# Kernel optimization log

Measured on AMD Instinct MI355X. Metric: run time of the kernel, lower is better.

The kernel has to match this reference:

```python
import jax, jax.numpy as jnp
import numpy as np

B, L, D, H, VOCAB = 8, 1024, 1024, 8, 32000
DH = D // H  # dim_per_head = 128
SCALE = float((DH // H) ** (-0.5))  # faithful to key.size(-1)//num_heads
EPS = 1e-5


def setup_inputs() -> dict:
    key = jax.random.key(0)
    ks = jax.random.split(key, 12)
    tokens = jax.random.randint(ks[0], (B, L), 0, VOCAB)
    s = 0.02
    emb = jax.random.normal(ks[1], (VOCAB, D), jnp.float32) * s
    emb = emb.at[0].set(0.0)  # padding_idx=0
    Wq = jax.random.normal(ks[2], (D, D), jnp.float32) * s
    Wk = jax.random.normal(ks[3], (D, D), jnp.float32) * s
    Wv = jax.random.normal(ks[4], (D, D), jnp.float32) * s
    Wo = jax.random.normal(ks[5], (D, D), jnp.float32) * s
    bq = jnp.zeros((D,), jnp.float32)
    bk = jnp.zeros((D,), jnp.float32)
    bv = jnp.zeros((D,), jnp.float32)
    bo = jnp.zeros((D,), jnp.float32)
    gamma = jnp.ones((2 * D,), jnp.float32)
    beta = jnp.zeros((2 * D,), jnp.float32)
    return {"tokens": tokens, "emb": emb, "Wq": Wq, "bq": bq, "Wk": Wk,
            "bk": bk, "Wv": Wv, "bv": bv, "Wo": Wo, "bo": bo,
            "gamma": gamma, "beta": beta}


def reference(tokens, emb, Wq, bq, Wk, bk, Wv, bv, Wo, bo, gamma, beta):
    # padding mask: [B, L, L] True where key token == 0
    pad = (tokens == 0)  # [B, L]
    mask = jnp.broadcast_to(pad[:, None, :], (B, L, L))
    mask = jnp.tile(mask, (H, 1, 1))  # torch .repeat(num_heads,1,1) -> [H*B, L, L]

    x = emb[tokens]  # [B, L, D]

    q = (x @ Wq + bq).reshape(B * H, L, DH)  # faithful interleaved view
    k = (x @ Wk + bk).reshape(B * H, L, DH)
    v = (x @ Wv + bv).reshape(B * H, L, DH)

    scores = jnp.einsum('bqd,bkd->bqk', q, k) * SCALE
    scores = jnp.where(mask, -jnp.inf, scores)
    attn = jax.nn.softmax(scores, axis=-1)
    ctx = jnp.einsum('bqk,bkd->bqd', attn, v).reshape(B, L, D)

    out = ctx @ Wo + bo  # [B, L, D]
    r = x + out
    maxpool = r.max(axis=1)   # [B, D]
    meanpool = r.mean(axis=1)  # [B, D]
    agg = jnp.concatenate([maxpool, meanpool], axis=1)  # [B, 2D]

    mu = agg.mean(axis=-1, keepdims=True)
    var = agg.var(axis=-1, keepdims=True)
    return (agg - mu) / jnp.sqrt(var + EPS) * gamma + beta
```

## Files before the change

### kernel.cpp

```cpp
#include <hip/hip_runtime.h>
#include <math.h>

typedef __attribute__((ext_vector_type(8))) short short8;
typedef __attribute__((ext_vector_type(4))) float f32x4;

constexpr int CB = 8, CL = 1024, CD = 1024, CDH = 128, CM = 8192;
constexpr float CSCALE = 0.25f;
constexpr float CEPS = 1e-5f;

__device__ inline ushort f2b(float f) {
    union { float f; unsigned u; } v; v.f = f;
    unsigned r = v.u + 0x7FFF + ((v.u >> 16) & 1);
    return (ushort)(r >> 16);
}
__device__ inline float b2f(ushort u) {
    union { unsigned u; float f; } v; v.u = ((unsigned)u) << 16;
    return v.f;
}

__device__ inline void gld16(const void* g, void* l) {
    __builtin_amdgcn_global_load_lds(
        (const __attribute__((address_space(1))) void*)g,
        (__attribute__((address_space(3))) void*)l, 16, 0, 0);
}

__global__ __launch_bounds__(256) void k_gather(const int* __restrict__ tokens,
                                                const float* __restrict__ emb,
                                                float* __restrict__ x,
                                                ushort* __restrict__ xb) {
    int row = blockIdx.x;
    int tok = tokens[row];
    float4 v = ((const float4*)(emb + (size_t)tok * CD))[threadIdx.x];
    ((float4*)(x + (size_t)row * CD))[threadIdx.x] = v;
    ushort4 o; o.x = f2b(v.x); o.y = f2b(v.y); o.z = f2b(v.z); o.w = f2b(v.w);
    ((ushort4*)(xb + (size_t)row * CD))[threadIdx.x] = o;
}

__global__ __launch_bounds__(256) void k_wtrans(const float* __restrict__ W,
                                                ushort* __restrict__ Wt) {
    __shared__ float ws_[32][33];
    const int tk = blockIdx.x * 32, tn = blockIdx.y * 32;
    const int t = threadIdx.x;
    {
        int r = t >> 3, c4 = (t & 7) * 4;
        *(float4*)&ws_[r][c4] = *(const float4*)&W[(size_t)(tk + r) * CD + tn + c4];
    }
    __syncthreads();
    int n = t >> 3, k4 = (t & 7) * 4;
    ushort4 o;
    o.x = f2b(ws_[k4 + 0][n]); o.y = f2b(ws_[k4 + 1][n]);
    o.z = f2b(ws_[k4 + 2][n]); o.w = f2b(ws_[k4 + 3][n]);
    *(ushort4*)&Wt[(size_t)(tn + n) * CD + tk + k4] = o;
}

__global__ __launch_bounds__(256) void k_gemm_qkv(const ushort* __restrict__ A,
                                                  const ushort* __restrict__ Wt3,
                                                  const float* __restrict__ b0,
                                                  const float* __restrict__ b1,
                                                  const float* __restrict__ b2,
                                                  ushort* __restrict__ C3) {
    __shared__ ushort As[128 * 32];
    __shared__ ushort Bs[128 * 32];
    const int z = blockIdx.z;
    const ushort* Bt  = Wt3 + (size_t)z * CD * CD;
    const float* bias = (z == 0) ? b0 : ((z == 1) ? b1 : b2);
    ushort* Cout      = C3 + (size_t)z * CM * CD;

    const int t = threadIdx.x, w = t >> 6, l = t & 63;
    const int lane15 = l & 15, quad = l >> 4;
    const int bm = blockIdx.y * 128, bn = blockIdx.x * 128;
    const int wm = (w >> 1) * 64, wn = (w & 1) * 64;
    const int arow = l >> 2;
    const int aseg = (l & 3) * 8;
    f32x4 acc[4][4] = {};

    for (int k0 = 0; k0 < CD; k0 += 32) {
        __syncthreads();
        #pragma unroll
        for (int c2 = 0; c2 < 2; ++c2) {
            int c = w * 2 + c2;
            gld16(A  + (size_t)(bm + c * 16 + arow) * CD + k0 + aseg, &As[c * 512 + l * 8]);
            gld16(Bt + (size_t)(bn + c * 16 + arow) * CD + k0 + aseg, &Bs[c * 512 + l * 8]);
        }
        __syncthreads();
        short8 af[4], bf[4];
        #pragma unroll
        for (int im = 0; im < 4; ++im)
            af[im] = *(const short8*)&As[(wm + im * 16 + lane15) * 32 + quad * 8];
        #pragma unroll
        for (int in = 0; in < 4; ++in)
            bf[in] = *(const short8*)&Bs[(wn + in * 16 + lane15) * 32 + quad * 8];
        #pragma unroll
        for (int im = 0; im < 4; ++im)
            #pragma unroll
            for (int in = 0; in < 4; ++in)
                acc[im][in] = __builtin_amdgcn_mfma_f32_16x16x32_bf16(af[im], bf[in], acc[im][in], 0, 0, 0);
    }
    #pragma unroll
    for (int in = 0; in < 4; ++in) {
        int col = bn + wn + in * 16 + lane15;
        float bv = bias[col];
        #pragma unroll
        for (int im = 0; im < 4; ++im) {
            int row0 = bm + wm + im * 16 + quad * 4;
            #pragma unroll
            for (int r = 0; r < 4; ++r)
                Cout[(size_t)(row0 + r) * CD + col] = f2b(acc[im][in][r] + bv);
        }
    }
}

__global__ __launch_bounds__(256) void k_gemm_out(const ushort* __restrict__ A,
                                                  const ushort* __restrict__ Bt,
                                                  const float* __restrict__ bias,
                                                  const float* __restrict__ resid,
                                                  float* __restrict__ Cout) {
    __shared__ ushort As[128 * 32];
    __shared__ ushort Bs[128 * 32];
    const int t = threadIdx.x, w = t >> 6, l = t & 63;
    const int lane15 = l & 15, quad = l >> 4;
    const int bm = blockIdx.y * 128, bn = blockIdx.x * 128;
    const int wm = (w >> 1) * 64, wn = (w & 1) * 64;
    const int arow = l >> 2;
    const int aseg = (l & 3) * 8;
    f32x4 acc[4][4] = {};

    for (int k0 = 0; k0 < CD; k0 += 32) {
        __syncthreads();
        #pragma unroll
        for (int c2 = 0; c2 < 2; ++c2) {
            int c = w * 2 + c2;
            gld16(A  + (size_t)(bm + c * 16 + arow) * CD + k0 + aseg, &As[c * 512 + l * 8]);
            gld16(Bt + (size_t)(bn + c * 16 + arow) * CD + k0 + aseg, &Bs[c * 512 + l * 8]);
        }
        __syncthreads();
        short8 af[4], bf[4];
        #pragma unroll
        for (int im = 0; im < 4; ++im)
            af[im] = *(const short8*)&As[(wm + im * 16 + lane15) * 32 + quad * 8];
        #pragma unroll
        for (int in = 0; in < 4; ++in)
            bf[in] = *(const short8*)&Bs[(wn + in * 16 + lane15) * 32 + quad * 8];
        #pragma unroll
        for (int im = 0; im < 4; ++im)
            #pragma unroll
            for (int in = 0; in < 4; ++in)
                acc[im][in] = __builtin_amdgcn_mfma_f32_16x16x32_bf16(af[im], bf[in], acc[im][in], 0, 0, 0);
    }
    #pragma unroll
    for (int in = 0; in < 4; ++in) {
        int col = bn + wn + in * 16 + lane15;
        float bv = bias[col];
        #pragma unroll
        for (int im = 0; im < 4; ++im) {
            int row0 = bm + wm + im * 16 + quad * 4;
            #pragma unroll
            for (int r = 0; r < 4; ++r) {
                size_t idx = (size_t)(row0 + r) * CD + col;
                Cout[idx] = acc[im][in][r] + bv + resid[idx];
            }
        }
    }
}

__global__ __launch_bounds__(256) void k_vtransp(const ushort* __restrict__ v,
                                                 ushort* __restrict__ Vtp) {
    __shared__ ushort Vs[64 * 136];
    const int i = blockIdx.x >> 4, kt = blockIdx.x & 15;
    const ushort* src = v + (size_t)i * 131072 + (size_t)kt * 64 * 128;
    const int t = threadIdx.x;
    #pragma unroll
    for (int ii = 0; ii < 4; ++ii) {
        int idx = t + 256 * ii;
        int key = idx >> 4, seg = idx & 15;
        *(uint4*)&Vs[key * 136 + seg * 8] = *(const uint4*)&src[key * 128 + seg * 8];
    }
    __syncthreads();
    ushort* dst = Vtp + (size_t)blockIdx.x * 8192;
    #pragma unroll
    for (int it = 0; it < 4; ++it) {
        int L = t + 256 * it;
        int cell = L & 63;
        int quadk = cell >> 4, l15 = cell & 15;
        int p = L >> 6;
        int d = (p >> 1) * 16 + l15;
        int kb = ((p & 1) * 4 + quadk) * 8;
        uint pk[4];
        #pragma unroll
        for (int jj = 0; jj < 4; ++jj) {
            uint lo = Vs[(kb + 2 * jj) * 136 + d];
            uint hi = Vs[(kb + 2 * jj + 1) * 136 + d];
            pk[jj] = lo | (hi << 16);
        }
        *(uint4*)&dst[(size_t)L * 8] = *(uint4*)pk;
    }
}

__global__ __launch_bounds__(512) void k_attn(const ushort* __restrict__ Q,
                                              const ushort* __restrict__ K,
                                              const ushort* __restrict__ Vtp,
                                              const int* __restrict__ tokens,
                                              ushort* __restrict__ ctx) {
    __shared__ ushort Ks[16 * 512];
    __shared__ ushort Vs[16 * 512];
    __shared__ ushort Ps[8 * 1088];
    __shared__ ushort Msk[CL];
    const int i = blockIdx.x, qb = blockIdx.y * 128;
    const int t = threadIdx.x, w = t >> 6, l = t & 63;
    const int lane15 = l & 15, quad = l >> 4;

    {
        const int* tokb = tokens + (i & 7) * CL;
        #pragma unroll
        for (int jj = 0; jj < 2; ++jj) {
            int idx = t + 512 * jj;
            Msk[idx] = (tokb[idx] == 0) ? (ushort)0xFF80 : (ushort)0;
        }
    }
    const int qrow = qb + w * 16 + lane15;
    short8 af[4];
    #pragma unroll
    for (int kc = 0; kc < 4; ++kc)
        af[kc] = *(const short8*)&Q[(size_t)i * 131072 + (size_t)qrow * 128 + kc * 32 + quad * 8];

    f32x4 oacc[8];
    #pragma unroll
    for (int dt = 0; dt < 8; ++dt) oacc[dt] = f32x4{0.f, 0.f, 0.f, 0.f};
    float lsum[4] = {0.f, 0.f, 0.f, 0.f};
    const int wbase = w * 1088;

    for (int kt = 0; kt < 16; ++kt) {
        __syncthreads();
        #pragma unroll
        for (int c = 0; c < 2; ++c) {
            int p = w * 2 + c;
            gld16(K + (size_t)i * 131072 + (size_t)(kt * 64 + (p >> 2) * 16 + lane15) * 128
                    + (p & 3) * 32 + quad * 8,
                  &Ks[p * 512 + l * 8]);
            gld16(Vtp + ((size_t)(i * 16 + kt) * 16 + p) * 512 + l * 8,
                  &Vs[p * 512 + l * 8]);
        }
        __syncthreads();

        f32x4 sc[4];
        #pragma unroll
        for (int j = 0; j < 4; ++j) {
            sc[j] = f32x4{0.f, 0.f, 0.f, 0.f};
            #pragma unroll
            for (int kc = 0; kc < 4; ++kc) {
                short8 bk = *(const short8*)&Ks[(j * 4 + kc) * 512 + l * 8];
                sc[j] = __builtin_amdgcn_mfma_f32_16x16x32_bf16(af[kc], bk, sc[j], 0, 0, 0);
            }
        }
        #pragma unroll
        for (int j = 0; j < 4; ++j) {
            float mj = b2f(Msk[kt * 64 + j * 16 + lane15]);
            #pragma unroll
            for (int r = 0; r < 4; ++r) {
                float p = __expf(fmaf(sc[j][r], CSCALE, mj));
                sc[j][r] = p;
                lsum[r] += p;
            }
        }
        #pragma unroll
        for (int j = 0; j < 4; ++j) {
            int ks2 = j >> 1;
            int qq  = (j & 1) * 2 + (lane15 >> 3);
            int pos = lane15 & 7;
            #pragma unroll
            for (int r = 0; r < 4; ++r) {
                union { float f; unsigned u; } cv; cv.f = sc[j][r];
                Ps[wbase + ks2 * 544 + qq * 136 + (quad * 4 + r) * 8 + pos] =
                    (ushort)(cv.u >> 16);
            }
        }
        short8 ap[2];
        #pragma unroll
        for (int ks2 = 0; ks2 < 2; ++ks2)
            ap[ks2] = *(const short8*)&Ps[wbase + ks2 * 544 + quad * 136 + lane15 * 8];
        #pragma unroll
        for (int dt = 0; dt < 8; ++dt)
            #pragma unroll
            for (int ks2 = 0; ks2 < 2; ++ks2) {
                short8 bv = *(const short8*)&Vs[(dt * 2 + ks2) * 512 + l * 8];
                oacc[dt] = __builtin_amdgcn_mfma_f32_16x16x32_bf16(ap[ks2], bv, oacc[dt], 0, 0, 0);
            }
    }
    float inv[4];
    #pragma unroll
    for (int r = 0; r < 4; ++r) {
        float s = lsum[r];
        #pragma unroll
        for (int off = 1; off < 16; off <<= 1) s += __shfl_xor(s, off);
        inv[r] = 1.f / s;
    }
    #pragma unroll
    for (int dt = 0; dt < 8; ++dt)
        #pragma unroll
        for (int r = 0; r < 4; ++r) {
            int q = qb + w * 16 + quad * 4 + r;
            ctx[(size_t)i * 131072 + (size_t)q * 128 + dt * 16 + lane15] =
                f2b(oacc[dt][r] * inv[r]);
        }
}

__global__ __launch_bounds__(256) void k_pool1(const float* __restrict__ R,
                                               float* __restrict__ pmax,
                                               float* __restrict__ psum) {
    const int chunk = blockIdx.x, b = blockIdx.y;
    const int d4 = threadIdx.x;
    const float4* base = (const float4*)(R + ((size_t)b * CL + chunk * 32) * CD) + d4;
    float4 mx = base[0];
    float4 sm = mx;
    for (int lr = 1; lr < 32; ++lr) {
        float4 v = base[(size_t)lr * (CD / 4)];
        mx.x = fmaxf(mx.x, v.x); mx.y = fmaxf(mx.y, v.y);
        mx.z = fmaxf(mx.z, v.z); mx.w = fmaxf(mx.w, v.w);
        sm.x += v.x; sm.y += v.y; sm.z += v.z; sm.w += v.w;
    }
    size_t off = ((size_t)b * 32 + chunk) * CD;
    ((float4*)(pmax + off))[d4] = mx;
    ((float4*)(psum + off))[d4] = sm;
}

__global__ __launch_bounds__(1024) void k_pool2(const float* __restrict__ pmax,
                                                const float* __restrict__ psum,
                                                const float* __restrict__ gamma,
                                                const float* __restrict__ beta,
                                                float* __restrict__ out) {
    __shared__ float rs[16], rq[16];
    __shared__ float s_mu, s_inv;
    const int b = blockIdx.x;
    const int d = threadIdx.x;
    float mx = -3.4e38f, sm = 0.f;
    for (int c = 0; c < 32; ++c) {
        size_t off = ((size_t)b * 32 + c) * CD + d;
        mx = fmaxf(mx, pmax[off]);
        sm += psum[off];
    }
    const float a0 = mx;
    const float a1 = sm * (1.0f / 1024.0f);
    float s = a0 + a1;
    float qd = a0 * a0 + a1 * a1;
    #pragma unroll
    for (int off = 32; off > 0; off >>= 1) {
        s  += __shfl_xor(s, off);
        qd += __shfl_xor(qd, off);
    }
    const int wid = d >> 6;
    if ((d & 63) == 0) { rs[wid] = s; rq[wid] = qd; }
    __syncthreads();
    if (d == 0) {
        float S = 0.f, Qm = 0.f;
        for (int ww = 0; ww < 16; ++ww) { S += rs[ww]; Qm += rq[ww]; }
        float mu  = S * (1.0f / 2048.0f);
        float var = Qm * (1.0f / 2048.0f) - mu * mu;
        s_mu = mu; s_inv = 1.0f / sqrtf(var + CEPS);
    }
    __syncthreads();
    const float mu = s_mu, inv = s_inv;
    out[(size_t)b * 2048 + d]        = (a0 - mu) * inv * gamma[d]        + beta[d];
    out[(size_t)b * 2048 + 1024 + d] = (a1 - mu) * inv * gamma[1024 + d] + beta[1024 + d];
}

extern "C" void kernel_launch(void* const* d_in, const int* in_sizes, int n_in,
                              void* d_out, int out_size, void* d_ws, size_t ws_size,
                              hipStream_t stream) {
    const int*   tokens = (const int*)d_in[0];
    const float* emb    = (const float*)d_in[1];
    const float* Wq     = (const float*)d_in[2];
    const float* bq     = (const float*)d_in[3];
    const float* Wk     = (const float*)d_in[4];
    const float* bk     = (const float*)d_in[5];
    const float* Wv     = (const float*)d_in[6];
    const float* bv     = (const float*)d_in[7];
    const float* Wo     = (const float*)d_in[8];
    const float* bo     = (const float*)d_in[9];
    const float* gamma  = (const float*)d_in[10];
    const float* beta   = (const float*)d_in[11];
    float* out = (float*)d_out;

    char* p = (char*)d_ws;
    float*  x   = (float*)p;   p += (size_t)CM * CD * 4;
    ushort* xb  = (ushort*)p;  p += (size_t)CM * CD * 2;
    ushort* wqt = (ushort*)p;  p += (size_t)CD * CD * 2;
    ushort* wkt = (ushort*)p;  p += (size_t)CD * CD * 2;
    ushort* wvt = (ushort*)p;  p += (size_t)CD * CD * 2;
    ushort* wot = (ushort*)p;  p += (size_t)CD * CD * 2;
    ushort* qb_ = (ushort*)p;  p += (size_t)CM * CD * 2;
    ushort* kb_ = (ushort*)p;  p += (size_t)CM * CD * 2;
    ushort* vb_ = (ushort*)p;  p += (size_t)CM * CD * 2;
    ushort* Vtp = (ushort*)p;  p += (size_t)CM * CD * 2;
    float*  pmax = (float*)p;  p += (size_t)CB * 32 * CD * 4;
    float*  psum = (float*)p;  p += (size_t)CB * 32 * CD * 4;
    float*  R   = (float*)qb_;
    ushort* ctx = vb_;

    k_gather<<<CM, 256, 0, stream>>>(tokens, emb, x, xb);

    dim3 wg(32, 32);
    k_wtrans<<<wg, 256, 0, stream>>>(Wq, wqt);
    k_wtrans<<<wg, 256, 0, stream>>>(Wk, wkt);
    k_wtrans<<<wg, 256, 0, stream>>>(Wv, wvt);
    k_wtrans<<<wg, 256, 0, stream>>>(Wo, wot);

    dim3 gq(CD / 128, CM / 128, 3);
    k_gemm_qkv<<<gq, 256, 0, stream>>>(xb, wqt, bq, bk, bv, qb_);

    k_vtransp<<<64 * 16, 256, 0, stream>>>(vb_, Vtp);

    dim3 ag(64, 8);
    k_attn<<<ag, 512, 0, stream>>>(qb_, kb_, Vtp, tokens, ctx);

    dim3 gg(CD / 128, CM / 128);
    k_gemm_out<<<gg, 256, 0, stream>>>(ctx, wot, bo, x, R);

    k_pool1<<<dim3(32, CB), 256, 0, stream>>>(R, pmax, psum);
    k_pool2<<<CB, 1024, 0, stream>>>(pmax, psum, gamma, beta, out);
}
```

Before: 383.0 us.

## Pipeline GEMMs with double-buffered LDS and fuse pooling into output GEMM

Both GEMMs move to 256x128 tiles with 512 threads, a double-buffered LDS pipeline that prefetches the next K slice while MFMAs run, and setprio around the MFMA block. The QKV GEMM flattens the z dimension into blockIdx.x, which relies on the three transposed weights being contiguous in memory. The output GEMM now reduces max and sum over its rows in the epilogue, so the fp32 residual tensor R is never written and pool1 is removed. The cost is more LDS and registers per block and hand-written waitcnt/barrier sequencing that has to be exactly right.

```diff
diff --git a/kernel.cpp b/kernel.cpp
--- a/kernel.cpp
+++ b/kernel.cpp
@@ -53,56 +53,89 @@
     *(ushort4*)&Wt[(size_t)(tn + n) * CD + tk + k4] = o;
 }
 
-__global__ __launch_bounds__(256) void k_gemm_qkv(const ushort* __restrict__ A,
-                                                  const ushort* __restrict__ Wt3,
-                                                  const float* __restrict__ b0,
-                                                  const float* __restrict__ b1,
-                                                  const float* __restrict__ b2,
-                                                  ushort* __restrict__ C3) {
-    __shared__ ushort As[128 * 32];
-    __shared__ ushort Bs[128 * 32];
-    const int z = blockIdx.z;
-    const ushort* Bt  = Wt3 + (size_t)z * CD * CD;
-    const float* bias = (z == 0) ? b0 : ((z == 1) ? b1 : b2);
-    ushort* Cout      = C3 + (size_t)z * CM * CD;
-
+__device__ inline void stage24(const ushort* __restrict__ A,
+                               const ushort* __restrict__ B,
+                               ushort* ldsA, ushort* ldsB,
+                               int bm, int bn, int kbase,
+                               int w, int lane15, int quad, int l) {
+    #pragma unroll
+    for (int c = 0; c < 3; ++c) {
+        int pid = w * 3 + c;
+        if (pid < 16)
+            gld16(A + (size_t)(bm + pid * 16 + lane15) * CD + kbase + quad * 8,
+                  ldsA + pid * 512 + (size_t)l * 8);
+        else
+            gld16(B + (size_t)(bn + (pid - 16) * 16 + lane15) * CD + kbase + quad * 8,
+                  ldsB + (pid - 16) * 512 + (size_t)l * 8);
+    }
+}
+
+#define GEMM_PIPELINE(Aptr, Bptr)                                                  \
+    f32x4 acc[4][4] = {};                                                          \
+    stage24(Aptr, Bptr, &As_[0][0][0][0], &Bs_[0][0][0][0], bm, bn, 0,             \
+            w, lane15, quad, l);                                                   \
+    stage24(Aptr, Bptr, &As_[0][1][0][0], &Bs_[0][1][0][0], bm, bn, 32,            \
+            w, lane15, quad, l);                                                   \
+    asm volatile("s_waitcnt vmcnt(3)" ::: "memory");                               \
+    __builtin_amdgcn_s_barrier();                                                  \
+    int cur = 0;                                                                   \
+    for (int kt = 0; kt < 16; ++kt) {                                              \
+        const int nk = (kt + 1) & 15;                                              \
+        _Pragma("unroll")                                                          \
+        for (int kh = 0; kh < 2; ++kh) {                                           \
+            short8 af[4], bf[4];                                                   \
+            _Pragma("unroll")                                                      \
+            for (int im = 0; im < 4; ++im)                                         \
+                af[im] = *(const short8*)&As_[cur][kh][wr * 4 + im][(size_t)l * 8];\
+            _Pragma("unroll")                                                      \
+            for (int in = 0; in < 4; ++in)                                         \
+                bf[in] = *(const short8*)&Bs_[cur][kh][wc * 4 + in][(size_t)l * 8];\
+            stage24(Aptr, Bptr, &As_[cur ^ 1][kh][0][0], &Bs_[cur ^ 1][kh][0][0],  \
+                    bm, bn, nk * 64 + kh * 32, w, lane15, quad, l);                \
+            __builtin_amdgcn_s_barrier();                                          \
+            asm volatile("s_waitcnt lgkmcnt(0)" ::: "memory");                     \
+            __builtin_amdgcn_s_setprio(1);                                         \
+            _Pragma("unroll")                                                      \
+            for (int im = 0; im < 4; ++im)                                         \
+                _Pragma("unroll")                                                  \
+                for (int in = 0; in < 4; ++in)                                     \
+                    acc[im][in] = __builtin_amdgcn_mfma_f32_16x16x32_bf16(         \
+                        af[im], bf[in], acc[im][in], 0, 0, 0);                     \
+            __builtin_amdgcn_s_setprio(0);                                         \
+            asm volatile("s_waitcnt vmcnt(3)" ::: "memory");                       \
+            __builtin_amdgcn_s_barrier();                                          \
+        }                                                                          \
+        cur ^= 1;                                                                  \
+    }                                                                              \
+    asm volatile("s_waitcnt vmcnt(0)" ::: "memory");
+
+__global__ __launch_bounds__(512, 2) void k_gemm_qkv(const ushort* __restrict__ A,
+                                                     const ushort* __restrict__ Wt3,
+                                                     const float* __restrict__ b0,
+                                                     const float* __restrict__ b1,
+                                                     const float* __restrict__ b2,
+                                                     ushort* __restrict__ C3) {
+    __shared__ ushort As_[2][2][16][512];
+    __shared__ ushort Bs_[2][2][8][512];
     const int t = threadIdx.x, w = t >> 6, l = t & 63;
     const int lane15 = l & 15, quad = l >> 4;
-    const int bm = blockIdx.y * 128, bn = blockIdx.x * 128;
-    const int wm = (w >> 1) * 64, wn = (w & 1) * 64;
-    const int arow = l >> 2;
-    const int aseg = (l & 3) * 8;
-    f32x4 acc[4][4] = {};
-
-    for (int k0 = 0; k0 < CD; k0 += 32) {
-        __syncthreads();
-        #pragma unroll
-        for (int c2 = 0; c2 < 2; ++c2) {
-            int c = w * 2 + c2;
-            gld16(A  + (size_t)(bm + c * 16 + arow) * CD + k0 + aseg, &As[c * 512 + l * 8]);
-            gld16(Bt + (size_t)(bn + c * 16 + arow) * CD + k0 + aseg, &Bs[c * 512 + l * 8]);
-        }
-        __syncthreads();
-        short8 af[4], bf[4];
-        #pragma unroll
-        for (int im = 0; im < 4; ++im)
-            af[im] = *(const short8*)&As[(wm + im * 16 + lane15) * 32 + quad * 8];
-        #pragma unroll
-        for (int in = 0; in < 4; ++in)
-            bf[in] = *(const short8*)&Bs[(wn + in * 16 + lane15) * 32 + quad * 8];
-        #pragma unroll
-        for (int im = 0; im < 4; ++im)
-            #pragma unroll
-            for (int in = 0; in < 4; ++in)
-                acc[im][in] = __builtin_amdgcn_mfma_f32_16x16x32_bf16(af[im], bf[in], acc[im][in], 0, 0, 0);
-    }
+    const int wr = w >> 1, wc = w & 1;
+    const int bx = blockIdx.x, by = blockIdx.y;
+    const int bm = by * 256, bn = bx * 128;
+
+    GEMM_PIPELINE(A, Wt3)
+
+    const int z = bx >> 3;
+    const float* bias = (z == 0) ? b0 : ((z == 1) ? b1 : b2);
+    ushort* Cout = C3 + (size_t)z * CM * CD;
+    const int colbase = (bx & 7) * 128 + wc * 64;
     #pragma unroll
     for (int in = 0; in < 4; ++in) {
-        int col = bn + wn + in * 16 + lane15;
+        int col = colbase + in * 16 + lane15;
         float bv = bias[col];
         #pragma unroll
         for (int im = 0; im < 4; ++im) {
-            int row0 = bm + wm + im * 16 + quad * 4;
+            int row0 = bm + wr * 64 + im * 16 + quad * 4;
             #pragma unroll
             for (int r = 0; r < 4; ++r)
                 Cout[(size_t)(row0 + r) * CD + col] = f2b(acc[im][in][r] + bv);
@@ -110,56 +143,65 @@
     }
 }
 
-__global__ __launch_bounds__(256) void k_gemm_out(const ushort* __restrict__ A,
-                                                  const ushort* __restrict__ Bt,
-                                                  const float* __restrict__ bias,
-                                                  const float* __restrict__ resid,
-                                                  float* __restrict__ Cout) {
-    __shared__ ushort As[128 * 32];
-    __shared__ ushort Bs[128 * 32];
+__global__ __launch_bounds__(512, 2) void k_gemm_out(const ushort* __restrict__ A,
+                                                     const ushort* __restrict__ Bt,
+                                                     const float* __restrict__ bias,
+                                                     const float* __restrict__ resid,
+                                                     float* __restrict__ pmax,
+                                                     float* __restrict__ psum) {
+    __shared__ ushort As_[2][2][16][512];
+    __shared__ ushort Bs_[2][2][8][512];
+    __shared__ float redmx[8][64], redsm[8][64];
     const int t = threadIdx.x, w = t >> 6, l = t & 63;
     const int lane15 = l & 15, quad = l >> 4;
-    const int bm = blockIdx.y * 128, bn = blockIdx.x * 128;
-    const int wm = (w >> 1) * 64, wn = (w & 1) * 64;
-    const int arow = l >> 2;
-    const int aseg = (l & 3) * 8;
-    f32x4 acc[4][4] = {};
-
-    for (int k0 = 0; k0 < CD; k0 += 32) {
-        __syncthreads();
-        #pragma unroll
-        for (int c2 = 0; c2 < 2; ++c2) {
-            int c = w * 2 + c2;
-            gld16(A  + (size_t)(bm + c * 16 + arow) * CD + k0 + aseg, &As[c * 512 + l * 8]);
-            gld16(Bt + (size_t)(bn + c * 16 + arow) * CD + k0 + aseg, &Bs[c * 512 + l * 8]);
-        }
-        __syncthreads();
-        short8 af[4], bf[4];
-        #pragma unroll
-        for (int im = 0; im < 4; ++im)
-            af[im] = *(const short8*)&As[(wm + im * 16 + lane15) * 32 + quad * 8];
-        #pragma unroll
-        for (int in = 0; in < 4; ++in)
-            bf[in] = *(const short8*)&Bs[(wn + in * 16 + lane15) * 32 + quad * 8];
-        #pragma unroll
-        for (int im = 0; im < 4; ++im)
-            #pragma unroll
-            for (int in = 0; in < 4; ++in)
-                acc[im][in] = __builtin_amdgcn_mfma_f32_16x16x32_bf16(af[im], bf[in], acc[im][in], 0, 0, 0);
-    }
+    const int wr = w >> 1, wc = w & 1;
+    const int bx = blockIdx.x, by = blockIdx.y;
+    const int bm = by * 256, bn = bx * 128;
+
+    GEMM_PIPELINE(A, Bt)
+
+    const int bb = by >> 2, chunk = by & 3;
+    float vmax_[4], vsum_[4];
     #pragma unroll
     for (int in = 0; in < 4; ++in) {
-        int col = bn + wn + in * 16 + lane15;
-        float bv = bias[col];
+        int col = bn + wc * 64 + in * 16 + lane15;
+        float bvv = bias[col];
+        float mx = -3.4e38f, sm = 0.f;
         #pragma unroll
         for (int im = 0; im < 4; ++im) {
-            int row0 = bm + wm + im * 16 + quad * 4;
+            int row0 = bm + wr * 64 + im * 16 + quad * 4;
             #pragma unroll
             for (int r = 0; r < 4; ++r) {
-                size_t idx = (size_t)(row0 + r) * CD + col;
-                Cout[idx] = acc[im][in][r] + bv + resid[idx];
+                float rel = acc[im][in][r] + bvv + resid[(size_t)(row0 + r) * CD + col];
+                mx = fmaxf(mx, rel);
+                sm += rel;
             }
         }
+        mx = fmaxf(mx, __shfl_xor(mx, 16));
+        mx = fmaxf(mx, __shfl_xor(mx, 32));
+        sm += __shfl_xor(sm, 16);
+        sm += __shfl_xor(sm, 32);
+        vmax_[in] = mx; vsum_[in] = sm;
+    }
+    if (l < 16) {
+        #pragma unroll
+        for (int in = 0; in < 4; ++in) {
+            redmx[w][in * 16 + lane15] = vmax_[in];
+            redsm[w][in * 16 + lane15] = vsum_[in];
+        }
+    }
+    __syncthreads();
+    if (t < 128) {
+        int wc2 = t >> 6, cc = t & 63;
+        float m = redmx[wc2][cc], s = redsm[wc2][cc];
+        #pragma unroll
+        for (int j = 1; j < 4; ++j) {
+            m = fmaxf(m, redmx[j * 2 + wc2][cc]);
+            s += redsm[j * 2 + wc2][cc];
+        }
+        size_t off = ((size_t)bb * 4 + chunk) * CD + bn + wc2 * 64 + cc;
+        pmax[off] = m;
+        psum[off] = s;
     }
 }
 
@@ -304,25 +346,6 @@
         }
 }
 
-__global__ __launch_bounds__(256) void k_pool1(const float* __restrict__ R,
-                                               float* __restrict__ pmax,
-                                               float* __restrict__ psum) {
-    const int chunk = blockIdx.x, b = blockIdx.y;
-    const int d4 = threadIdx.x;
-    const float4* base = (const float4*)(R + ((size_t)b * CL + chunk * 32) * CD) + d4;
-    float4 mx = base[0];
-    float4 sm = mx;
-    for (int lr = 1; lr < 32; ++lr) {
-        float4 v = base[(size_t)lr * (CD / 4)];
-        mx.x = fmaxf(mx.x, v.x); mx.y = fmaxf(mx.y, v.y);
-        mx.z = fmaxf(mx.z, v.z); mx.w = fmaxf(mx.w, v.w);
-        sm.x += v.x; sm.y += v.y; sm.z += v.z; sm.w += v.w;
-    }
-    size_t off = ((size_t)b * 32 + chunk) * CD;
-    ((float4*)(pmax + off))[d4] = mx;
-    ((float4*)(psum + off))[d4] = sm;
-}
-
 __global__ __launch_bounds__(1024) void k_pool2(const float* __restrict__ pmax,
                                                 const float* __restrict__ psum,
                                                 const float* __restrict__ gamma,
@@ -333,8 +356,9 @@
     const int b = blockIdx.x;
     const int d = threadIdx.x;
     float mx = -3.4e38f, sm = 0.f;
-    for (int c = 0; c < 32; ++c) {
-        size_t off = ((size_t)b * 32 + c) * CD + d;
+    #pragma unroll
+    for (int c = 0; c < 4; ++c) {
+        size_t off = ((size_t)b * 4 + c) * CD + d;
         mx = fmaxf(mx, pmax[off]);
         sm += psum[off];
     }
@@ -391,9 +415,8 @@
     ushort* kb_ = (ushort*)p;  p += (size_t)CM * CD * 2;
     ushort* vb_ = (ushort*)p;  p += (size_t)CM * CD * 2;
     ushort* Vtp = (ushort*)p;  p += (size_t)CM * CD * 2;
-    float*  pmax = (float*)p;  p += (size_t)CB * 32 * CD * 4;
-    float*  psum = (float*)p;  p += (size_t)CB * 32 * CD * 4;
-    float*  R   = (float*)qb_;
+    float*  pmax = (float*)p;  p += (size_t)CB * 4 * CD * 4;
+    float*  psum = (float*)p;  p += (size_t)CB * 4 * CD * 4;
     ushort* ctx = vb_;
 
     k_gather<<<CM, 256, 0, stream>>>(tokens, emb, x, xb);
@@ -404,17 +427,16 @@
     k_wtrans<<<wg, 256, 0, stream>>>(Wv, wvt);
     k_wtrans<<<wg, 256, 0, stream>>>(Wo, wot);
 
-    dim3 gq(CD / 128, CM / 128, 3);
-    k_gemm_qkv<<<gq, 256, 0, stream>>>(xb, wqt, bq, bk, bv, qb_);
+    dim3 gq(3 * CD / 128, CM / 256);
+    k_gemm_qkv<<<gq, 512, 0, stream>>>(xb, wqt, bq, bk, bv, qb_);
 
     k_vtransp<<<64 * 16, 256, 0, stream>>>(vb_, Vtp);
 
     dim3 ag(64, 8);
     k_attn<<<ag, 512, 0, stream>>>(qb_, kb_, Vtp, tokens, ctx);
 
-    dim3 gg(CD / 128, CM / 128);
-    k_gemm_out<<<gg, 256, 0, stream>>>(ctx, wot, bo, x, R);
-
-    k_pool1<<<dim3(32, CB), 256, 0, stream>>>(R, pmax, psum);
+    dim3 go(CD / 128, CM / 256);
+    k_gemm_out<<<go, 512, 0, stream>>>(ctx, wot, bo, x, pmax, psum);
+
     k_pool2<<<CB, 1024, 0, stream>>>(pmax, psum, gamma, beta, out);
 }
```

After: 379.5 us. Within noise of the previous version (-0.9%).

## Fuse max/mean pooling into output GEMM epilogue and remap GEMM tiles per XCD

Applied to the files above, without the earlier changes.

The output projection GEMM now reduces its residual-added tile directly into per-chunk max and sum partials using shuffles and shared memory. This removes the full fp32 R write and the separate pool1 pass that re-read it. Both GEMMs switch to a 1D grid with an XCD-aware block-to-tile mapping meant to improve L2 locality. The QKV GEMM treats the three weight matrices as one wide N=3072 operand, and the LDS fill is reordered so fragment reads are contiguous per lane. The trade-offs are a heavier GEMM epilogue and possible LDS bank conflicts from the new layout.

```diff
diff --git a/kernel.cpp b/kernel.cpp
--- a/kernel.cpp
+++ b/kernel.cpp
@@ -53,25 +53,24 @@
     *(ushort4*)&Wt[(size_t)(tn + n) * CD + tk + k4] = o;
 }
 
+
 __global__ __launch_bounds__(256) void k_gemm_qkv(const ushort* __restrict__ A,
                                                   const ushort* __restrict__ Wt3,
                                                   const float* __restrict__ b0,
                                                   const float* __restrict__ b1,
                                                   const float* __restrict__ b2,
                                                   ushort* __restrict__ C3) {
-    __shared__ ushort As[128 * 32];
-    __shared__ ushort Bs[128 * 32];
-    const int z = blockIdx.z;
-    const ushort* Bt  = Wt3 + (size_t)z * CD * CD;
-    const float* bias = (z == 0) ? b0 : ((z == 1) ? b1 : b2);
-    ushort* Cout      = C3 + (size_t)z * CM * CD;
-
+    __shared__ ushort As[8 * 512];
+    __shared__ ushort Bs[8 * 512];
     const int t = threadIdx.x, w = t >> 6, l = t & 63;
     const int lane15 = l & 15, quad = l >> 4;
-    const int bm = blockIdx.y * 128, bn = blockIdx.x * 128;
-    const int wm = (w >> 1) * 64, wn = (w & 1) * 64;
-    const int arow = l >> 2;
-    const int aseg = (l & 3) * 8;
+    const int wr = w >> 1, wc = w & 1;
+    const int wm = wr * 64, wn = wc * 64;
+    const int id = blockIdx.x;
+    const int xcd = id & 7, off = id >> 3;
+    const int bxt = (xcd & 1) * 12 + off % 12;
+    const int by  = (xcd >> 1) * 16 + off / 12;
+    const int bm = by * 128, bn = bxt * 128;
     f32x4 acc[4][4] = {};
 
     for (int k0 = 0; k0 < CD; k0 += 32) {
@@ -79,26 +78,32 @@
         #pragma unroll
         for (int c2 = 0; c2 < 2; ++c2) {
             int c = w * 2 + c2;
-            gld16(A  + (size_t)(bm + c * 16 + arow) * CD + k0 + aseg, &As[c * 512 + l * 8]);
-            gld16(Bt + (size_t)(bn + c * 16 + arow) * CD + k0 + aseg, &Bs[c * 512 + l * 8]);
+            gld16(A   + (size_t)(bm + c * 16 + lane15) * CD + k0 + quad * 8,
+                  &As[c * 512 + l * 8]);
+            gld16(Wt3 + (size_t)(bn + c * 16 + lane15) * CD + k0 + quad * 8,
+                  &Bs[c * 512 + l * 8]);
         }
         __syncthreads();
         short8 af[4], bf[4];
         #pragma unroll
         for (int im = 0; im < 4; ++im)
-            af[im] = *(const short8*)&As[(wm + im * 16 + lane15) * 32 + quad * 8];
+            af[im] = *(const short8*)&As[(wr * 4 + im) * 512 + l * 8];
         #pragma unroll
         for (int in = 0; in < 4; ++in)
-            bf[in] = *(const short8*)&Bs[(wn + in * 16 + lane15) * 32 + quad * 8];
+            bf[in] = *(const short8*)&Bs[(wc * 4 + in) * 512 + l * 8];
         #pragma unroll
         for (int im = 0; im < 4; ++im)
             #pragma unroll
             for (int in = 0; in < 4; ++in)
                 acc[im][in] = __builtin_amdgcn_mfma_f32_16x16x32_bf16(af[im], bf[in], acc[im][in], 0, 0, 0);
     }
+    const int z = bn >> 10;
+    const float* bias = (z == 0) ? b0 : ((z == 1) ? b1 : b2);
+    ushort* Cout = C3 + (size_t)z * CM * CD;
+    const int colbase = (bn & 1023) + wn;
     #pragma unroll
     for (int in = 0; in < 4; ++in) {
-        int col = bn + wn + in * 16 + lane15;
+        int col = colbase + in * 16 + lane15;
         float bv = bias[col];
         #pragma unroll
         for (int im = 0; im < 4; ++im) {
@@ -114,15 +119,20 @@
                                                   const ushort* __restrict__ Bt,
                                                   const float* __restrict__ bias,
                                                   const float* __restrict__ resid,
-                                                  float* __restrict__ Cout) {
-    __shared__ ushort As[128 * 32];
-    __shared__ ushort Bs[128 * 32];
+                                                  float* __restrict__ pmax,
+                                                  float* __restrict__ psum) {
+    __shared__ ushort As[8 * 512];
+    __shared__ ushort Bs[8 * 512];
+    __shared__ float redmx[4][64], redsm[4][64];
     const int t = threadIdx.x, w = t >> 6, l = t & 63;
     const int lane15 = l & 15, quad = l >> 4;
-    const int bm = blockIdx.y * 128, bn = blockIdx.x * 128;
-    const int wm = (w >> 1) * 64, wn = (w & 1) * 64;
-    const int arow = l >> 2;
-    const int aseg = (l & 3) * 8;
+    const int wr = w >> 1, wc = w & 1;
+    const int wm = wr * 64, wn = wc * 64;
+    const int id = blockIdx.x;
+    const int xcd = id & 7, off = id >> 3;
+    const int bx = off & 7;
+    const int by = xcd * 8 + (off >> 3);
+    const int bm = by * 128, bn = bx * 128;
     f32x4 acc[4][4] = {};
 
     for (int k0 = 0; k0 < CD; k0 += 32) {
@@ -130,36 +140,63 @@
         #pragma unroll
         for (int c2 = 0; c2 < 2; ++c2) {
             int c = w * 2 + c2;
-            gld16(A  + (size_t)(bm + c * 16 + arow) * CD + k0 + aseg, &As[c * 512 + l * 8]);
-            gld16(Bt + (size_t)(bn + c * 16 + arow) * CD + k0 + aseg, &Bs[c * 512 + l * 8]);
+            gld16(A  + (size_t)(bm + c * 16 + lane15) * CD + k0 + quad * 8,
+                  &As[c * 512 + l * 8]);
+            gld16(Bt + (size_t)(bn + c * 16 + lane15) * CD + k0 + quad * 8,
+                  &Bs[c * 512 + l * 8]);
         }
         __syncthreads();
         short8 af[4], bf[4];
         #pragma unroll
         for (int im = 0; im < 4; ++im)
-            af[im] = *(const short8*)&As[(wm + im * 16 + lane15) * 32 + quad * 8];
+            af[im] = *(const short8*)&As[(wr * 4 + im) * 512 + l * 8];
         #pragma unroll
         for (int in = 0; in < 4; ++in)
-            bf[in] = *(const short8*)&Bs[(wn + in * 16 + lane15) * 32 + quad * 8];
+            bf[in] = *(const short8*)&Bs[(wc * 4 + in) * 512 + l * 8];
         #pragma unroll
         for (int im = 0; im < 4; ++im)
             #pragma unroll
             for (int in = 0; in < 4; ++in)
                 acc[im][in] = __builtin_amdgcn_mfma_f32_16x16x32_bf16(af[im], bf[in], acc[im][in], 0, 0, 0);
     }
+    const int bb = by >> 3, chunk = by & 7;
+    float vmax_[4], vsum_[4];
     #pragma unroll
     for (int in = 0; in < 4; ++in) {
         int col = bn + wn + in * 16 + lane15;
-        float bv = bias[col];
+        float bvv = bias[col];
+        float mx = -3.4e38f, sm = 0.f;
         #pragma unroll
         for (int im = 0; im < 4; ++im) {
             int row0 = bm + wm + im * 16 + quad * 4;
             #pragma unroll
             for (int r = 0; r < 4; ++r) {
-                size_t idx = (size_t)(row0 + r) * CD + col;
-                Cout[idx] = acc[im][in][r] + bv + resid[idx];
+                float rel = acc[im][in][r] + bvv + resid[(size_t)(row0 + r) * CD + col];
+                mx = fmaxf(mx, rel);
+                sm += rel;
             }
         }
+        mx = fmaxf(mx, __shfl_xor(mx, 16));
+        mx = fmaxf(mx, __shfl_xor(mx, 32));
+        sm += __shfl_xor(sm, 16);
+        sm += __shfl_xor(sm, 32);
+        vmax_[in] = mx; vsum_[in] = sm;
+    }
+    if (l < 16) {
+        #pragma unroll
+        for (int in = 0; in < 4; ++in) {
+            redmx[w][in * 16 + lane15] = vmax_[in];
+            redsm[w][in * 16 + lane15] = vsum_[in];
+        }
+    }
+    __syncthreads();
+    if (t < 128) {
+        int wcol = t >> 6, cc = t & 63;
+        float m = fmaxf(redmx[wcol][cc], redmx[wcol + 2][cc]);
+        float s = redsm[wcol][cc] + redsm[wcol + 2][cc];
+        size_t off2 = ((size_t)bb * 8 + chunk) * CD + bn + wcol * 64 + cc;
+        pmax[off2] = m;
+        psum[off2] = s;
     }
 }
 
@@ -304,25 +341,6 @@
         }
 }
 
-__global__ __launch_bounds__(256) void k_pool1(const float* __restrict__ R,
-                                               float* __restrict__ pmax,
-                                               float* __restrict__ psum) {
-    const int chunk = blockIdx.x, b = blockIdx.y;
-    const int d4 = threadIdx.x;
-    const float4* base = (const float4*)(R + ((size_t)b * CL + chunk * 32) * CD) + d4;
-    float4 mx = base[0];
-    float4 sm = mx;
-    for (int lr = 1; lr < 32; ++lr) {
-        float4 v = base[(size_t)lr * (CD / 4)];
-        mx.x = fmaxf(mx.x, v.x); mx.y = fmaxf(mx.y, v.y);
-        mx.z = fmaxf(mx.z, v.z); mx.w = fmaxf(mx.w, v.w);
-        sm.x += v.x; sm.y += v.y; sm.z += v.z; sm.w += v.w;
-    }
-    size_t off = ((size_t)b * 32 + chunk) * CD;
-    ((float4*)(pmax + off))[d4] = mx;
-    ((float4*)(psum + off))[d4] = sm;
-}
-
 __global__ __launch_bounds__(1024) void k_pool2(const float* __restrict__ pmax,
                                                 const float* __restrict__ psum,
                                                 const float* __restrict__ gamma,
@@ -333,8 +351,9 @@
     const int b = blockIdx.x;
     const int d = threadIdx.x;
     float mx = -3.4e38f, sm = 0.f;
-    for (int c = 0; c < 32; ++c) {
-        size_t off = ((size_t)b * 32 + c) * CD + d;
+    #pragma unroll
+    for (int c = 0; c < 8; ++c) {
+        size_t off = ((size_t)b * 8 + c) * CD + d;
         mx = fmaxf(mx, pmax[off]);
         sm += psum[off];
     }
@@ -391,9 +410,8 @@
     ushort* kb_ = (ushort*)p;  p += (size_t)CM * CD * 2;
     ushort* vb_ = (ushort*)p;  p += (size_t)CM * CD * 2;
     ushort* Vtp = (ushort*)p;  p += (size_t)CM * CD * 2;
-    float*  pmax = (float*)p;  p += (size_t)CB * 32 * CD * 4;
-    float*  psum = (float*)p;  p += (size_t)CB * 32 * CD * 4;
-    float*  R   = (float*)qb_;
+    float*  pmax = (float*)p;  p += (size_t)CB * 8 * CD * 4;
+    float*  psum = (float*)p;  p += (size_t)CB * 8 * CD * 4;
     ushort* ctx = vb_;
 
     k_gather<<<CM, 256, 0, stream>>>(tokens, emb, x, xb);
@@ -404,17 +422,14 @@
     k_wtrans<<<wg, 256, 0, stream>>>(Wv, wvt);
     k_wtrans<<<wg, 256, 0, stream>>>(Wo, wot);
 
-    dim3 gq(CD / 128, CM / 128, 3);
-    k_gemm_qkv<<<gq, 256, 0, stream>>>(xb, wqt, bq, bk, bv, qb_);
+    k_gemm_qkv<<<1536, 256, 0, stream>>>(xb, wqt, bq, bk, bv, qb_);
 
     k_vtransp<<<64 * 16, 256, 0, stream>>>(vb_, Vtp);
 
     dim3 ag(64, 8);
     k_attn<<<ag, 512, 0, stream>>>(qb_, kb_, Vtp, tokens, ctx);
 
-    dim3 gg(CD / 128, CM / 128);
-    k_gemm_out<<<gg, 256, 0, stream>>>(ctx, wot, bo, x, R);
-
-    k_pool1<<<dim3(32, CB), 256, 0, stream>>>(R, pmax, psum);
+    k_gemm_out<<<512, 256, 0, stream>>>(ctx, wot, bo, x, pmax, psum);
+
     k_pool2<<<CB, 1024, 0, stream>>>(pmax, psum, gamma, beta, out);
 }
```

Result: slower. 398.6 us (+4.1%).

## Fuse max/mean pooling partials into output projection GEMM epilogue

Applied to the files above, without the earlier changes.

The output GEMM epilogue now reduces its residual-added tile over rows to per-column max and sum partials, using shuffles and shared memory, and writes those partials directly. This removes the full fp32 R write (32 MB), its re-read in the separate pool1 kernel, and one launch. pool2 now combines 8 partial chunks per batch instead of 32. The cost is extra reduction work, shared memory and a barrier in the GEMM epilogue.

```diff
diff --git a/kernel.cpp b/kernel.cpp
--- a/kernel.cpp
+++ b/kernel.cpp
@@ -114,9 +114,11 @@
                                                   const ushort* __restrict__ Bt,
                                                   const float* __restrict__ bias,
                                                   const float* __restrict__ resid,
-                                                  float* __restrict__ Cout) {
+                                                  float* __restrict__ pmax,
+                                                  float* __restrict__ psum) {
     __shared__ ushort As[128 * 32];
     __shared__ ushort Bs[128 * 32];
+    __shared__ float redmx[4][64], redsm[4][64];
     const int t = threadIdx.x, w = t >> 6, l = t & 63;
     const int lane15 = l & 15, quad = l >> 4;
     const int bm = blockIdx.y * 128, bn = blockIdx.x * 128;
@@ -147,19 +149,44 @@
             for (int in = 0; in < 4; ++in)
                 acc[im][in] = __builtin_amdgcn_mfma_f32_16x16x32_bf16(af[im], bf[in], acc[im][in], 0, 0, 0);
     }
+    const int by = blockIdx.y, bb = by >> 3, chunk = by & 7;
+    float vmax_[4], vsum_[4];
     #pragma unroll
     for (int in = 0; in < 4; ++in) {
         int col = bn + wn + in * 16 + lane15;
-        float bv = bias[col];
+        float bvv = bias[col];
+        float mx = -3.4e38f, sm = 0.f;
         #pragma unroll
         for (int im = 0; im < 4; ++im) {
             int row0 = bm + wm + im * 16 + quad * 4;
             #pragma unroll
             for (int r = 0; r < 4; ++r) {
-                size_t idx = (size_t)(row0 + r) * CD + col;
-                Cout[idx] = acc[im][in][r] + bv + resid[idx];
+                float rel = acc[im][in][r] + bvv + resid[(size_t)(row0 + r) * CD + col];
+                mx = fmaxf(mx, rel);
+                sm += rel;
             }
         }
+        mx = fmaxf(mx, __shfl_xor(mx, 16));
+        mx = fmaxf(mx, __shfl_xor(mx, 32));
+        sm += __shfl_xor(sm, 16);
+        sm += __shfl_xor(sm, 32);
+        vmax_[in] = mx; vsum_[in] = sm;
+    }
+    if (l < 16) {
+        #pragma unroll
+        for (int in = 0; in < 4; ++in) {
+            redmx[w][in * 16 + lane15] = vmax_[in];
+            redsm[w][in * 16 + lane15] = vsum_[in];
+        }
+    }
+    __syncthreads();
+    if (t < 128) {
+        int wcol = t >> 6, cc = t & 63;
+        float m = fmaxf(redmx[wcol][cc], redmx[wcol + 2][cc]);
+        float s = redsm[wcol][cc] + redsm[wcol + 2][cc];
+        size_t off2 = ((size_t)bb * 8 + chunk) * CD + bn + wcol * 64 + cc;
+        pmax[off2] = m;
+        psum[off2] = s;
     }
 }
 
@@ -304,25 +331,6 @@
         }
 }
 
-__global__ __launch_bounds__(256) void k_pool1(const float* __restrict__ R,
-                                               float* __restrict__ pmax,
-                                               float* __restrict__ psum) {
-    const int chunk = blockIdx.x, b = blockIdx.y;
-    const int d4 = threadIdx.x;
-    const float4* base = (const float4*)(R + ((size_t)b * CL + chunk * 32) * CD) + d4;
-    float4 mx = base[0];
-    float4 sm = mx;
-    for (int lr = 1; lr < 32; ++lr) {
-        float4 v = base[(size_t)lr * (CD / 4)];
-        mx.x = fmaxf(mx.x, v.x); mx.y = fmaxf(mx.y, v.y);
-        mx.z = fmaxf(mx.z, v.z); mx.w = fmaxf(mx.w, v.w);
-        sm.x += v.x; sm.y += v.y; sm.z += v.z; sm.w += v.w;
-    }
-    size_t off = ((size_t)b * 32 + chunk) * CD;
-    ((float4*)(pmax + off))[d4] = mx;
-    ((float4*)(psum + off))[d4] = sm;
-}
-
 __global__ __launch_bounds__(1024) void k_pool2(const float* __restrict__ pmax,
                                                 const float* __restrict__ psum,
                                                 const float* __restrict__ gamma,
@@ -333,8 +341,9 @@
     const int b = blockIdx.x;
     const int d = threadIdx.x;
     float mx = -3.4e38f, sm = 0.f;
-    for (int c = 0; c < 32; ++c) {
-        size_t off = ((size_t)b * 32 + c) * CD + d;
+    #pragma unroll
+    for (int c = 0; c < 8; ++c) {
+        size_t off = ((size_t)b * 8 + c) * CD + d;
         mx = fmaxf(mx, pmax[off]);
         sm += psum[off];
     }
@@ -391,9 +400,8 @@
     ushort* kb_ = (ushort*)p;  p += (size_t)CM * CD * 2;
     ushort* vb_ = (ushort*)p;  p += (size_t)CM * CD * 2;
     ushort* Vtp = (ushort*)p;  p += (size_t)CM * CD * 2;
-    float*  pmax = (float*)p;  p += (size_t)CB * 32 * CD * 4;
-    float*  psum = (float*)p;  p += (size_t)CB * 32 * CD * 4;
-    float*  R   = (float*)qb_;
+    float*  pmax = (float*)p;  p += (size_t)CB * 8 * CD * 4;
+    float*  psum = (float*)p;  p += (size_t)CB * 8 * CD * 4;
     ushort* ctx = vb_;
 
     k_gather<<<CM, 256, 0, stream>>>(tokens, emb, x, xb);
@@ -412,9 +420,8 @@
     dim3 ag(64, 8);
     k_attn<<<ag, 512, 0, stream>>>(qb_, kb_, Vtp, tokens, ctx);
 
-    dim3 gg(CD / 128, CM / 128);
-    k_gemm_out<<<gg, 256, 0, stream>>>(ctx, wot, bo, x, R);
-
-    k_pool1<<<dim3(32, CB), 256, 0, stream>>>(R, pmax, psum);
+    dim3 go(CD / 128, CM / 128);
+    k_gemm_out<<<go, 256, 0, stream>>>(ctx, wot, bo, x, pmax, psum);
+
     k_pool2<<<CB, 1024, 0, stream>>>(pmax, psum, gamma, beta, out);
 }
```

Result: faster. 366.2 us (-4.4%).
